# Optimization experiments

Measured on AMD Instinct MI355X. Metric: run time of the kernel, lower is better.

## Reference

```python
import jax, jax.numpy as jnp
import numpy as np

HK, WK = 7, 11  # local_k


def _local_mask(H, W):
    # Equivalent to the torch buffer: 0 inside the hk x wk window centered on the
    # query position (for odd hk, wk), -inf outside. Shape (N, N), N = H*W.
    n = jnp.arange(H * W)
    hq, wq = n // W, n % W
    dh = jnp.abs(hq[:, None] - hq[None, :])
    dw = jnp.abs(wq[:, None] - wq[None, :])
    allowed = (dh <= HK // 2) & (dw <= WK // 2)
    return jnp.where(allowed, 0.0, -jnp.inf).astype(jnp.float32)


def setup_inputs() -> dict:
    key = jax.random.key(0)
    k1, k2, k3 = jax.random.split(key, 3)
    B, H, W, C = 8, 32, 64, 512
    N = H * W
    x = jax.random.normal(k1, (B, N, C), dtype=jnp.float32)
    qkv_w = jax.random.normal(k2, (3 * C, C), dtype=jnp.float32) * (C ** -0.5)
    proj_w = jax.random.normal(k3, (C, C), dtype=jnp.float32) * (C ** -0.5)
    proj_b = jnp.zeros((C,), dtype=jnp.float32)
    return {"x": x, "qkv_w": qkv_w, "proj_w": proj_w, "proj_b": proj_b, "H": H, "W": W}


def reference(x, qkv_w, proj_w, proj_b, H, W):
    B, N, C = x.shape
    num_heads = 8
    head_dim = C // num_heads
    scale = head_dim ** -0.5

    # qkv: Linear(dim, 3*dim, bias=False) -> (B, N, 3, heads, head_dim)
    qkv = (x @ qkv_w.T).reshape(B, N, 3, num_heads, head_dim)
    q = qkv[:, :, 0].transpose(0, 2, 1, 3) * scale  # (B, h, N, d)
    k = qkv[:, :, 1].transpose(0, 2, 1, 3)
    v = qkv[:, :, 2].transpose(0, 2, 1, 3)

    attn = jnp.einsum('bhnd,bhmd->bhnm', q, k)  # (B, h, N, N)
    attn = attn + _local_mask(H, W)  # broadcast over (B, h)
    attn = jax.nn.softmax(attn, axis=-1)

    out = jnp.einsum('bhnm,bhmd->bhnd', attn, v)  # (B, h, N, d)
    out = out.transpose(0, 2, 1, 3).reshape(B, N, C)
    return out @ proj_w.T + proj_b
```

## Files before the change

### kernel.cpp

```cpp
#include <hip/hip_runtime.h>
#include <hip/hip_bf16.h>

#define B_SZ 8
#define H_SZ 32
#define W_SZ 64
#define N_SZ 2048
#define C_SZ 512
#define NH 8
#define HD 64

using u16 = unsigned short;
typedef __attribute__((ext_vector_type(8))) short s16x8;
typedef __attribute__((ext_vector_type(4))) float f32x4;

__device__ __forceinline__ float bf2f(u16 u) {
    union { unsigned int i; float f; } c; c.i = ((unsigned int)u) << 16; return c.f;
}
__device__ __forceinline__ u16 f2bf(float f) {
    union { float f; unsigned int i; } c; c.f = f;
    unsigned int r = c.i + 0x7fffu + ((c.i >> 16) & 1u);
    return (u16)(r >> 16);
}

#define GLL16(gp, lp) __builtin_amdgcn_global_load_lds( \
    (const __attribute__((address_space(1))) unsigned int*)(gp), \
    (__attribute__((address_space(3))) unsigned int*)(lp), 16, 0, 0)

__device__ __forceinline__ int lds_off(int row, int chunk) {
    return (row * 8 + (chunk ^ (row & 7))) * 8;
}
__device__ __forceinline__ int lds_off32(int row, int chunk) {
    return (row * 4 + (chunk ^ (row & 3))) * 8;
}

#define NX4 2097152
#define NQ4 196608
#define NP4 65536
__global__ __launch_bounds__(256)
void conv_all(const float* __restrict__ x, const float* __restrict__ qw,
              const float* __restrict__ pw, u16* __restrict__ xb,
              u16* __restrict__ qwb, u16* __restrict__ pwb)
{
    const int i = blockIdx.x * 256 + threadIdx.x;
    const float* src; u16* dst; int idx; float sc = 1.0f;
    if (i < NX4)             { src = x;  dst = xb;  idx = i; }
    else if (i < NX4 + NQ4)  { src = qw; dst = qwb; idx = i - NX4;
                               if (idx < 65536) sc = 0.125f; }
    else                     { src = pw; dst = pwb; idx = i - NX4 - NQ4; }
    const float4 v = ((const float4*)src)[idx];
    ushort4 o = { f2bf(v.x * sc), f2bf(v.y * sc), f2bf(v.z * sc), f2bf(v.w * sc) };
    ((ushort4*)dst)[idx] = o;
}

template<int MODE, int NB>
__global__ __launch_bounds__(512, 4)
void gemm3(const u16* __restrict__ A, const u16* __restrict__ Bw,
           const float* __restrict__ bias,
           u16* __restrict__ q_ws, u16* __restrict__ k_ws, u16* __restrict__ v_ws,
           float* __restrict__ outp)
{
    __shared__ u16 As[3][256 * 32];
    __shared__ u16 Bs[3][128 * 32];
    const int t = threadIdx.x;
    const int chunk = gridDim.x >> 3;
    const int wg = (blockIdx.x & 7) * chunk + (blockIdx.x >> 3);
    const int m0 = (wg / NB) * 256;
    const int n0 = (wg % NB) * 128;
    const int wave = t >> 6, lane = t & 63;
    const int wm = (wave >> 2) * 128;
    const int wn = (wave & 3) * 32;
    const int l16 = lane & 15, quad = lane >> 4;
    const int srow = t >> 2;
    const int sch  = (t & 3) ^ (srow & 3);

    const u16* Ab = A  + (size_t)(m0 + srow) * C_SZ + sch * 8;
    const u16* Bb = Bw + (size_t)(n0 + srow) * C_SZ + sch * 8;

    f32x4 acc[8][2] = {};

    #pragma unroll
    for (int tb = 0; tb < 2; ++tb) {
        GLL16(Ab + tb * 32,                       &As[tb][t * 8]);
        GLL16(Ab + (size_t)128 * C_SZ + tb * 32,  &As[tb][4096 + t * 8]);
        GLL16(Bb + tb * 32,                       &Bs[tb][t * 8]);
    }

    #pragma unroll
    for (int tt = 0; tt < 16; ++tt) {
        const int cb = tt % 3;
        if (tt < 15) asm volatile("s_waitcnt vmcnt(3)" ::: "memory");
        else         asm volatile("s_waitcnt vmcnt(0)" ::: "memory");
        __builtin_amdgcn_s_barrier();
        __builtin_amdgcn_sched_barrier(0);

        if (tt < 14) {
            const int nb = (tt + 2) % 3;
            const int k0 = (tt + 2) * 32;
            GLL16(Ab + k0,                         &As[nb][t * 8]);
            GLL16(Ab + (size_t)128 * C_SZ + k0,    &As[nb][4096 + t * 8]);
            GLL16(Bb + k0,                         &Bs[nb][t * 8]);
        }

        s16x8 af0[4], bf[2];
        #pragma unroll
        for (int i = 0; i < 4; ++i)
            af0[i] = *(const s16x8*)&As[cb][lds_off32(wm + 16 * i + l16, quad)];
        #pragma unroll
        for (int j = 0; j < 2; ++j)
            bf[j] = *(const s16x8*)&Bs[cb][lds_off32(wn + 16 * j + l16, quad)];
        asm volatile("s_waitcnt lgkmcnt(0)" ::: "memory");
        __builtin_amdgcn_sched_barrier(0);
        __builtin_amdgcn_s_setprio(1);
        #pragma unroll
        for (int i = 0; i < 4; ++i)
            #pragma unroll
            for (int j = 0; j < 2; ++j)
                acc[i][j] = __builtin_amdgcn_mfma_f32_16x16x32_bf16(af0[i], bf[j], acc[i][j], 0, 0, 0);
        __builtin_amdgcn_s_setprio(0);

        s16x8 af1[4];
        #pragma unroll
        for (int i = 0; i < 4; ++i)
            af1[i] = *(const s16x8*)&As[cb][lds_off32(wm + 64 + 16 * i + l16, quad)];
        asm volatile("s_waitcnt lgkmcnt(0)" ::: "memory");
        __builtin_amdgcn_sched_barrier(0);
        __builtin_amdgcn_s_setprio(1);
        #pragma unroll
        for (int i = 0; i < 4; ++i)
            #pragma unroll
            for (int j = 0; j < 2; ++j)
                acc[4 + i][j] = __builtin_amdgcn_mfma_f32_16x16x32_bf16(af1[i], bf[j], acc[4 + i][j], 0, 0, 0);
        __builtin_amdgcn_s_setprio(0);
    }

    if (MODE == 0) {
        const int bb  = m0 >> 11;
        const int nnb = (m0 & 2047) + wm + (quad << 2);
        if (n0 >= 1024) {
            #pragma unroll
            for (int j = 0; j < 2; ++j) {
                const int c  = n0 - 1024 + wn + 16 * j + l16;
                const int h  = c >> 6, dd = c & 63;
                u16* vp = v_ws + (((size_t)bb * NH + h) * HD + dd) * N_SZ + nnb;
                #pragma unroll
                for (int i = 0; i < 8; ++i) {
                    ushort4 st = { f2bf(acc[i][j][0]), f2bf(acc[i][j][1]),
                                   f2bf(acc[i][j][2]), f2bf(acc[i][j][3]) };
                    *(ushort4*)(vp + 16 * i) = st;
                }
            }
        } else {
            u16* T = (n0 < 512) ? q_ws : k_ws;
            const int nq = n0 & 511;
            #pragma unroll
            for (int j = 0; j < 2; ++j) {
                const int gn = nq + wn + 16 * j + l16;
                const int h  = gn >> 6, dd = gn & 63;
                u16* tp = T + (((size_t)bb * NH + h) * N_SZ + nnb) * HD + dd;
                #pragma unroll
                for (int i = 0; i < 8; ++i)
                    #pragma unroll
                    for (int r = 0; r < 4; ++r)
                        tp[(size_t)(16 * i + r) * HD] = f2bf(acc[i][j][r]);
            }
        }
    } else {
        #pragma unroll
        for (int j = 0; j < 2; ++j) {
            const int gn = n0 + wn + 16 * j + l16;
            const float bv = bias[gn];
            #pragma unroll
            for (int i = 0; i < 8; ++i)
                #pragma unroll
                for (int r = 0; r < 4; ++r)
                    outp[(size_t)(m0 + wm + 16 * i + (quad << 2) + r) * C_SZ + gn]
                        = acc[i][j][r] + bv;
        }
    }
}

__global__ __launch_bounds__(256)
void attn_mfma(const u16* __restrict__ q_ws, const u16* __restrict__ k_ws,
               const u16* __restrict__ vt_ws, u16* __restrict__ o_ws)
{
    __shared__ u16 KV[2][64 * 64];
    __shared__ u16 Ps[4][16 * 40];

    const int t = threadIdx.x, wave = t >> 6, lane = t & 63;
    const int l16 = lane & 15, quad = lane >> 4;
    const int u  = blockIdx.x;
    const int p  = u & 15;
    const int bh = u >> 4;
    const int r0 = 2 * p, r1 = 2 * p + 1;
    const size_t base = (size_t)bh * (N_SZ * HD);
    const int srow = t >> 3;
    const int sch  = (t & 7) ^ (srow & 7);

    const u16* qg = q_ws + base + (size_t)r0 * (64 * HD);
    u16* Qst = &KV[0][0];
    #pragma unroll
    for (int g = 0; g < 4; ++g)
        GLL16(qg + (size_t)(srow + 32 * g) * 64 + sch * 8, Qst + g * 2048 + t * 8);
    __syncthreads();

    s16x8 aQ[2][2];
    #pragma unroll
    for (int s = 0; s < 2; ++s) {
        const int Rq = 64 * s + 16 * wave + l16;
        aQ[s][0] = *(const s16x8*)&Qst[lds_off(Rq, quad)];
        aQ[s][1] = *(const s16x8*)&Qst[lds_off(Rq, 4 + quad)];
    }

    const int kb = min(max(16 * wave - 8, 0), 32);

    f32x4 accO[2][4] = {};
    float lp[2][4] = {};

    const int hlo = (r0 - 3 < 0) ? 0 : r0 - 3;
    const int hhi = (r1 + 3 > H_SZ - 1) ? H_SZ - 1 : r1 + 3;

    for (int hh = hlo; hh <= hhi; ++hh) {
        __syncthreads();
        const u16* kg = k_ws + base + (size_t)hh * (64 * HD);
        GLL16(kg + (size_t)srow        * 64 + sch * 8, &KV[0][t * 8]);
        GLL16(kg + (size_t)(srow + 32) * 64 + sch * 8, &KV[0][2048 + t * 8]);
        const u16* vg = vt_ws + base + (size_t)hh * 64;
        GLL16(vg + (size_t)srow        * N_SZ + sch * 8, &KV[1][t * 8]);
        GLL16(vg + (size_t)(srow + 32) * N_SZ + sch * 8, &KV[1][2048 + t * 8]);
        __syncthreads();

        s16x8 bK[2][2];
        #pragma unroll
        for (int j = 0; j < 2; ++j) {
            const int Rk = kb + 16 * j + l16;
            bK[j][0] = *(const s16x8*)&KV[0][lds_off(Rk, quad)];
            bK[j][1] = *(const s16x8*)&KV[0][lds_off(Rk, 4 + quad)];
        }
        s16x8 vf[4];
        #pragma unroll
        for (int j = 0; j < 4; ++j)
            vf[j] = *(const s16x8*)&KV[1][lds_off(16 * j + l16, (kb >> 3) + quad)];

        #pragma unroll
        for (int s = 0; s < 2; ++s) {
            const int dh = hh - (r0 + s);
            if (dh * dh > 9) continue;
            f32x4 z[2] = {{0.f,0.f,0.f,0.f},{0.f,0.f,0.f,0.f}};
            #pragma unroll
            for (int j = 0; j < 2; ++j) {
                z[j] = __builtin_amdgcn_mfma_f32_16x16x32_bf16(aQ[s][0], bK[j][0], z[j], 0, 0, 0);
                z[j] = __builtin_amdgcn_mfma_f32_16x16x32_bf16(aQ[s][1], bK[j][1], z[j], 0, 0, 0);
            }
            #pragma unroll
            for (int j = 0; j < 2; ++j) {
                const int ww = kb + 16 * j + l16;
                #pragma unroll
                for (int r = 0; r < 4; ++r) {
                    const int dw = ww - (16 * wave + quad * 4 + r);
                    const float pv = (dw * dw <= 25) ? __expf(z[j][r]) : 0.f;
                    const u16 pb = f2bf(pv);
                    lp[s][r] += bf2f(pb);
                    Ps[wave][(quad * 4 + r) * 40 + 16 * j + l16] = pb;
                }
            }
            s16x8 aP = *(const s16x8*)&Ps[wave][l16 * 40 + quad * 8];
            #pragma unroll
            for (int j = 0; j < 4; ++j)
                accO[s][j] = __builtin_amdgcn_mfma_f32_16x16x32_bf16(aP, vf[j], accO[s][j], 0, 0, 0);
        }
    }

    #pragma unroll
    for (int s = 0; s < 2; ++s)
        #pragma unroll
        for (int r = 0; r < 4; ++r) {
            lp[s][r] += __shfl_xor(lp[s][r], 1);
            lp[s][r] += __shfl_xor(lp[s][r], 2);
            lp[s][r] += __shfl_xor(lp[s][r], 4);
            lp[s][r] += __shfl_xor(lp[s][r], 8);
        }

    const int bb = bh >> 3, h = bh & 7;
    #pragma unroll
    for (int s = 0; s < 2; ++s)
        #pragma unroll
        for (int j = 0; j < 4; ++j)
            #pragma unroll
            for (int r = 0; r < 4; ++r) {
                const int row = (r0 + s) * 64 + 16 * wave + quad * 4 + r;
                o_ws[((size_t)bb * N_SZ + row) * C_SZ + h * 64 + 16 * j + l16]
                    = f2bf(accO[s][j][r] / lp[s][r]);
            }
}

extern "C" void kernel_launch(void* const* d_in, const int* in_sizes, int n_in,
                              void* d_out, int out_size, void* d_ws, size_t ws_size,
                              hipStream_t stream)
{
    const float* x      = (const float*)d_in[0];
    const float* qkv_w  = (const float*)d_in[1];
    const float* proj_w = (const float*)d_in[2];
    const float* proj_b = (const float*)d_in[3];
    float* outp = (float*)d_out;

    const size_t seg = (size_t)B_SZ * NH * N_SZ * HD;
    u16* q_ws = (u16*)d_ws;
    u16* k_ws = q_ws + seg;
    u16* v_ws = k_ws + seg;
    u16* o_ws = v_ws + seg;
    u16* xb   = o_ws + seg;
    u16* qwb  = xb + (size_t)16384 * 512;
    u16* pwb  = qwb + (size_t)1536 * 512;

    conv_all<<<9216, 256, 0, stream>>>(x, qkv_w, proj_w, xb, qwb, pwb);

    gemm3<0, 12><<<768, 512, 0, stream>>>(xb, qwb, nullptr,
                                          q_ws, k_ws, v_ws, nullptr);
    attn_mfma<<<B_SZ * NH * (H_SZ / 2), 256, 0, stream>>>(q_ws, k_ws, v_ws, o_ws);
    gemm3<1, 4><<<256, 512, 0, stream>>>(o_ws, pwb, proj_b,
                                         nullptr, nullptr, nullptr, outp);
}
```

Measured before the change: 177.7 us.

## Double GEMM K-tile to 64 and split loads across two sub-phases

The GEMM K-step grows from 32 to 64, cutting the main loop from 16 to 8 iterations, and the LDS swizzle moves to an 8-chunk layout. Each iteration's global-to-LDS prefetch is split into two halves, each issued alongside one half of the MFMA work, with barriers around each phase. This aims to cut per-iteration sync and waitcnt overhead and hide more load latency. LDS use doubles to 144 KB per block and the occupancy hint of 4 is removed, so fewer blocks fit per CU.

```diff
diff --git a/kernel.cpp b/kernel.cpp
--- a/kernel.cpp
+++ b/kernel.cpp
@@ -28,9 +28,6 @@
 
 __device__ __forceinline__ int lds_off(int row, int chunk) {
     return (row * 8 + (chunk ^ (row & 7))) * 8;
-}
-__device__ __forceinline__ int lds_off32(int row, int chunk) {
-    return (row * 4 + (chunk ^ (row & 3))) * 8;
 }
 
 #define NX4 2097152
@@ -53,14 +50,14 @@
 }
 
 template<int MODE, int NB>
-__global__ __launch_bounds__(512, 4)
-void gemm3(const u16* __restrict__ A, const u16* __restrict__ Bw,
+__global__ __launch_bounds__(512)
+void gemm9(const u16* __restrict__ A, const u16* __restrict__ Bw,
            const float* __restrict__ bias,
            u16* __restrict__ q_ws, u16* __restrict__ k_ws, u16* __restrict__ v_ws,
            float* __restrict__ outp)
 {
-    __shared__ u16 As[3][256 * 32];
-    __shared__ u16 Bs[3][128 * 32];
+    __shared__ u16 As[3][256 * 64];
+    __shared__ u16 Bs[3][128 * 64];
     const int t = threadIdx.x;
     const int chunk = gridDim.x >> 3;
     const int wg = (blockIdx.x & 7) * chunk + (blockIdx.x >> 3);
@@ -70,68 +67,93 @@
     const int wm = (wave >> 2) * 128;
     const int wn = (wave & 3) * 32;
     const int l16 = lane & 15, quad = lane >> 4;
-    const int srow = t >> 2;
-    const int sch  = (t & 3) ^ (srow & 3);
+    const int srow = t >> 3;
+    const int sch  = (t & 7) ^ (srow & 7);
 
     const u16* Ab = A  + (size_t)(m0 + srow) * C_SZ + sch * 8;
     const u16* Bb = Bw + (size_t)(n0 + srow) * C_SZ + sch * 8;
 
     f32x4 acc[8][2] = {};
 
+#define SA(b, k0, g) GLL16(Ab + (size_t)(64 * (g)) * C_SZ + (k0), \
+                           &As[b][(g) * 4096 + t * 8])
+#define SB(b, k0, g) GLL16(Bb + (size_t)(64 * (g)) * C_SZ + (k0), \
+                           &Bs[b][(g) * 4096 + t * 8])
+
     #pragma unroll
     for (int tb = 0; tb < 2; ++tb) {
-        GLL16(Ab + tb * 32,                       &As[tb][t * 8]);
-        GLL16(Ab + (size_t)128 * C_SZ + tb * 32,  &As[tb][4096 + t * 8]);
-        GLL16(Bb + tb * 32,                       &Bs[tb][t * 8]);
-    }
-
-    #pragma unroll
-    for (int tt = 0; tt < 16; ++tt) {
-        const int cb = tt % 3;
-        if (tt < 15) asm volatile("s_waitcnt vmcnt(3)" ::: "memory");
-        else         asm volatile("s_waitcnt vmcnt(0)" ::: "memory");
+        SA(tb, tb * 64, 0); SA(tb, tb * 64, 1); SA(tb, tb * 64, 2); SA(tb, tb * 64, 3);
+        SB(tb, tb * 64, 0); SB(tb, tb * 64, 1);
+    }
+    asm volatile("s_waitcnt vmcnt(6)" ::: "memory");
+    __builtin_amdgcn_s_barrier();
+    __builtin_amdgcn_sched_barrier(0);
+
+    #pragma unroll
+    for (int tt = 0; tt < 8; ++tt) {
+        const int ct = tt % 3;
+        const int nt = (tt + 2) % 3;
+        const int k2 = (tt + 2) * 64;
+
+        s16x8 af[4][2], bf[2][2];
+        #pragma unroll
+        for (int i = 0; i < 4; ++i) {
+            const int R = wm + 16 * i + l16;
+            af[i][0] = *(const s16x8*)&As[ct][lds_off(R, quad)];
+            af[i][1] = *(const s16x8*)&As[ct][lds_off(R, 4 + quad)];
+        }
+        #pragma unroll
+        for (int j = 0; j < 2; ++j) {
+            const int R = wn + 16 * j + l16;
+            bf[j][0] = *(const s16x8*)&Bs[ct][lds_off(R, quad)];
+            bf[j][1] = *(const s16x8*)&Bs[ct][lds_off(R, 4 + quad)];
+        }
+        if (tt < 6) { SA(nt, k2, 0); SA(nt, k2, 1); SB(nt, k2, 0); }
+        __builtin_amdgcn_sched_barrier(0);
         __builtin_amdgcn_s_barrier();
-        __builtin_amdgcn_sched_barrier(0);
-
-        if (tt < 14) {
-            const int nb = (tt + 2) % 3;
-            const int k0 = (tt + 2) * 32;
-            GLL16(Ab + k0,                         &As[nb][t * 8]);
-            GLL16(Ab + (size_t)128 * C_SZ + k0,    &As[nb][4096 + t * 8]);
-            GLL16(Bb + k0,                         &Bs[nb][t * 8]);
-        }
-
-        s16x8 af0[4], bf[2];
+        asm volatile("s_waitcnt lgkmcnt(0)" ::: "memory");
+        __builtin_amdgcn_sched_barrier(0);
+        __builtin_amdgcn_s_setprio(1);
         #pragma unroll
         for (int i = 0; i < 4; ++i)
-            af0[i] = *(const s16x8*)&As[cb][lds_off32(wm + 16 * i + l16, quad)];
-        #pragma unroll
-        for (int j = 0; j < 2; ++j)
-            bf[j] = *(const s16x8*)&Bs[cb][lds_off32(wn + 16 * j + l16, quad)];
+            #pragma unroll
+            for (int j = 0; j < 2; ++j) {
+                acc[i][j] = __builtin_amdgcn_mfma_f32_16x16x32_bf16(af[i][0], bf[j][0], acc[i][j], 0, 0, 0);
+                acc[i][j] = __builtin_amdgcn_mfma_f32_16x16x32_bf16(af[i][1], bf[j][1], acc[i][j], 0, 0, 0);
+            }
+        __builtin_amdgcn_s_setprio(0);
+        __builtin_amdgcn_sched_barrier(0);
+        __builtin_amdgcn_s_barrier();
+        __builtin_amdgcn_sched_barrier(0);
+
+        #pragma unroll
+        for (int i = 0; i < 4; ++i) {
+            const int R = wm + 64 + 16 * i + l16;
+            af[i][0] = *(const s16x8*)&As[ct][lds_off(R, quad)];
+            af[i][1] = *(const s16x8*)&As[ct][lds_off(R, 4 + quad)];
+        }
+        if (tt < 6) { SA(nt, k2, 2); SA(nt, k2, 3); SB(nt, k2, 1); }
+        if (tt < 6)       asm volatile("s_waitcnt vmcnt(6)" ::: "memory");
+        else if (tt == 6) asm volatile("s_waitcnt vmcnt(0)" ::: "memory");
+        __builtin_amdgcn_sched_barrier(0);
+        __builtin_amdgcn_s_barrier();
         asm volatile("s_waitcnt lgkmcnt(0)" ::: "memory");
         __builtin_amdgcn_sched_barrier(0);
         __builtin_amdgcn_s_setprio(1);
         #pragma unroll
         for (int i = 0; i < 4; ++i)
             #pragma unroll
-            for (int j = 0; j < 2; ++j)
-                acc[i][j] = __builtin_amdgcn_mfma_f32_16x16x32_bf16(af0[i], bf[j], acc[i][j], 0, 0, 0);
+            for (int j = 0; j < 2; ++j) {
+                acc[4 + i][j] = __builtin_amdgcn_mfma_f32_16x16x32_bf16(af[i][0], bf[j][0], acc[4 + i][j], 0, 0, 0);
+                acc[4 + i][j] = __builtin_amdgcn_mfma_f32_16x16x32_bf16(af[i][1], bf[j][1], acc[4 + i][j], 0, 0, 0);
+            }
         __builtin_amdgcn_s_setprio(0);
-
-        s16x8 af1[4];
-        #pragma unroll
-        for (int i = 0; i < 4; ++i)
-            af1[i] = *(const s16x8*)&As[cb][lds_off32(wm + 64 + 16 * i + l16, quad)];
-        asm volatile("s_waitcnt lgkmcnt(0)" ::: "memory");
-        __builtin_amdgcn_sched_barrier(0);
-        __builtin_amdgcn_s_setprio(1);
-        #pragma unroll
-        for (int i = 0; i < 4; ++i)
-            #pragma unroll
-            for (int j = 0; j < 2; ++j)
-                acc[4 + i][j] = __builtin_amdgcn_mfma_f32_16x16x32_bf16(af1[i], bf[j], acc[4 + i][j], 0, 0, 0);
-        __builtin_amdgcn_s_setprio(0);
-    }
+        __builtin_amdgcn_sched_barrier(0);
+        __builtin_amdgcn_s_barrier();
+        __builtin_amdgcn_sched_barrier(0);
+    }
+#undef SA
+#undef SB
 
     if (MODE == 0) {
         const int bb  = m0 >> 11;
@@ -155,7 +177,7 @@
             #pragma unroll
             for (int j = 0; j < 2; ++j) {
                 const int gn = nq + wn + 16 * j + l16;
-                const int h  = gn >> 6, dd = gn & 63;
+                const int h  = (gn >> 6) & 7, dd = gn & 63;
                 u16* tp = T + (((size_t)bb * NH + h) * N_SZ + nnb) * HD + dd;
                 #pragma unroll
                 for (int i = 0; i < 8; ++i)
@@ -314,9 +336,9 @@
 
     conv_all<<<9216, 256, 0, stream>>>(x, qkv_w, proj_w, xb, qwb, pwb);
 
-    gemm3<0, 12><<<768, 512, 0, stream>>>(xb, qwb, nullptr,
+    gemm9<0, 12><<<768, 512, 0, stream>>>(xb, qwb, nullptr,
                                           q_ws, k_ws, v_ws, nullptr);
     attn_mfma<<<B_SZ * NH * (H_SZ / 2), 256, 0, stream>>>(q_ws, k_ws, v_ws, o_ws);
-    gemm3<1, 4><<<256, 512, 0, stream>>>(o_ws, pwb, proj_b,
+    gemm9<1, 4><<<256, 512, 0, stream>>>(o_ws, pwb, proj_b,
                                          nullptr, nullptr, nullptr, outp);
 }
```

Result: no change. 177.0 us (-0.4%).
